# Kernel tuning notes

Hardware: AMD Instinct MI355X
Metric: run time of the kernel (lower is better)

## Reference

```python
import jax, jax.numpy as jnp
import numpy as np

B, N, D, H = 2, 1536, 1024, 16
DH = D // H
SCALE = DH ** -0.5


def setup_inputs() -> dict:
    key = jax.random.key(0)
    ks = jax.random.split(key, 16)
    s = D ** -0.5
    x = jax.random.normal(ks[0], (B, N, D), dtype=jnp.float32)
    # causal prior: 0 on/below diagonal, -1e9 above
    causal = jnp.tril(jnp.ones((N, N), dtype=bool))
    attn_bias = jnp.where(causal, 0.0, -1e9).astype(jnp.float32)[None, None]
    mk = lambda k, shp: jax.random.normal(k, shp, dtype=jnp.float32) * s
    return {
        "x": x,
        "attn_bias": attn_bias,
        "Wq": mk(ks[1], (D, D)), "bq": jnp.zeros((D,), jnp.float32),
        "Wk": mk(ks[2], (D, D)), "bk": jnp.zeros((D,), jnp.float32),
        "Wv": mk(ks[3], (D, D)), "bv": jnp.zeros((D,), jnp.float32),
        "Wg1": mk(ks[4], (D, D)), "bg1": jnp.zeros((D,), jnp.float32),
        "Wg2": mk(ks[5], (D, 1)), "bg2": jnp.zeros((1,), jnp.float32),
        "Wo": mk(ks[6], (D, D)), "bo": jnp.zeros((D,), jnp.float32),
    }


def reference(x, attn_bias, Wq, bq, Wk, bk, Wv, bv, Wg1, bg1, Wg2, bg2, Wo, bo):
    b, n, d = x.shape
    # projections -> [B, H, N, DH]
    split = lambda t: t.reshape(b, n, H, DH).swapaxes(1, 2)
    Q = split(x @ Wq + bq)
    K = split(x @ Wk + bk)
    V = split(x @ Wv + bv)
    # scores [B, H, N, N]
    attn = jnp.einsum("bhnd,bhmd->bhnm", Q, K) * SCALE + attn_bias
    attn = jax.nn.softmax(attn, axis=-1)
    # per-(batch, head, query) entropy over key axis
    entropy = -(attn * jnp.log(attn + 1e-6)).sum(-1)  # [B, H, N]
    # gate MLP (torch nn.GELU default is exact erf)
    gate = jax.nn.sigmoid(jax.nn.gelu(x @ Wg1 + bg1, approximate=False) @ Wg2 + bg2)  # [B, N, 1]
    attn = attn * gate[:, None, :, :]  # broadcast over heads, keys
    out = jnp.einsum("bhnm,bhmd->bhnd", attn, V)
    out = out.swapaxes(1, 2).reshape(b, n, d) @ Wo + bo
    return out, entropy
```

## Files before the change

### kernel.cpp

```cpp
#include <hip/hip_runtime.h>
#include <hip/hip_bf16.h>
#include <math.h>

#define Bsz  2
#define Nseq 1536
#define Dmod 1024
#define NH   16
#define DHd  64
#define MTOT (Bsz*Nseq)
#define SCALE 0.125f
#define BK   32

typedef short  short8 __attribute__((ext_vector_type(8)));
typedef float  f32x4  __attribute__((ext_vector_type(4)));
typedef unsigned short u16x4 __attribute__((ext_vector_type(4)));
typedef unsigned short ushortT;

__device__ __forceinline__ float b2f(__hip_bfloat16 v) { return __bfloat162float(v); }
__device__ __forceinline__ unsigned short f2bf(float f) {
    union { float f; unsigned u; } a; a.f = f;
    unsigned r = a.u + 0x7fffu + ((a.u >> 16) & 1u);
    return (unsigned short)(r >> 16);
}

__device__ __forceinline__ void gl2lds16(const ushortT* g, ushortT* lds) {
    __builtin_amdgcn_global_load_lds(
        (const __attribute__((address_space(1))) unsigned int*)(g),
        (__attribute__((address_space(3))) unsigned int*)(lds),
        16, 0, 0);
}

__global__ __launch_bounds__(256)
void prep_kernel(const float* W0, const float* W1, const float* W2,
                 const float* W3, const float* W4,
                 ushortT* T0, ushortT* T1, ushortT* T2, ushortT* T3, ushortT* T4,
                 const float* __restrict__ x, ushortT* __restrict__ xb,
                 float* __restrict__ glogit)
{
    const int z = blockIdx.z;
    const int t = threadIdx.x;
    if (z == 5) {
        const int bi = blockIdx.y * 16 + blockIdx.x;
        const size_t NEl = (size_t)MTOT * Dmod;
        for (size_t i = ((size_t)bi * 256 + t) * 4; i < NEl; i += (size_t)256 * 256 * 4) {
            float4 v = *(const float4*)(x + i);
            u16x4 o = { f2bf(v.x), f2bf(v.y), f2bf(v.z), f2bf(v.w) };
            *(u16x4*)(xb + i) = o;
        }
        if (t < 12) glogit[bi * 12 + t] = 0.f;
        return;
    }
    __shared__ float tile[64][65];
    const float* W = z == 0 ? W0 : z == 1 ? W1 : z == 2 ? W2 : z == 3 ? W3 : W4;
    ushortT*     T = z == 0 ? T0 : z == 1 ? T1 : z == 2 ? T2 : z == 3 ? T3 : T4;
    const int k0 = blockIdx.x * 64, n0 = blockIdx.y * 64;
    for (int i = t; i < 4096; i += 256) {
        int r = i >> 6, c = i & 63;
        tile[r][c] = W[(size_t)(k0 + r) * 1024 + n0 + c];
    }
    __syncthreads();
    for (int i = t; i < 4096; i += 256) {
        int rn = i >> 6, ck = i & 63;
        T[(size_t)(n0 + rn) * 1024 + k0 + ck] = f2bf(tile[ck][rn]);
    }
}

__device__ __forceinline__
void gemm_core(const ushortT* __restrict__ A, const ushortT* __restrict__ Bt,
               int m0, int n0, ushortT* AsU, ushortT* BsU, f32x4 (&acc)[4][4])
{
    const int t = threadIdx.x;
    const int l = t & 63, w = t >> 6;
    const int wm = (w >> 1) * 64, wn = (w & 1) * 64;
    const int lm = l & 15, q = l >> 4;

    const int r0 = t >> 2, c0 = (t & 3) * 8;
    const ushortT* Ag0 = A  + (size_t)(m0 + r0) * 1024 + c0;
    const ushortT* Ag1 = Ag0 + (size_t)64 * 1024;
    const ushortT* Bg0 = Bt + (size_t)(n0 + r0) * 1024 + c0;
    const ushortT* Bg1 = Bg0 + (size_t)64 * 1024;
    ushortT* La0 = AsU + t * 8;
    ushortT* La1 = AsU + 2048 + t * 8;
    ushortT* Lb0 = BsU + t * 8;
    ushortT* Lb1 = BsU + 2048 + t * 8;

    for (int k0 = 0; k0 < 1024; k0 += BK) {
        gl2lds16(Ag0 + k0, La0);
        gl2lds16(Ag1 + k0, La1);
        gl2lds16(Bg0 + k0, Lb0);
        gl2lds16(Bg1 + k0, Lb1);
        __syncthreads();
        short8 af[4], bf[4];
#pragma unroll
        for (int i = 0; i < 4; ++i) {
            af[i] = *(const short8*)&AsU[(wm + i * 16 + lm) * 32 + q * 8];
            bf[i] = *(const short8*)&BsU[(wn + i * 16 + lm) * 32 + q * 8];
        }
#pragma unroll
        for (int i = 0; i < 4; ++i)
#pragma unroll
            for (int j = 0; j < 4; ++j)
                acc[i][j] = __builtin_amdgcn_mfma_f32_16x16x32_bf16(af[i], bf[j], acc[i][j], 0, 0, 0);
        __syncthreads();
    }
}

__global__ __launch_bounds__(256)
void gemm_qkvg(const ushortT* __restrict__ xb,
               const ushortT* Wt0, const ushortT* Wt1, const ushortT* Wt2, const ushortT* Wt3,
               const float* bz0, const float* bz1, const float* bz2, const float* bz3,
               const float* __restrict__ Wg2,
               ushortT* O0, ushortT* O1, ushortT* O2, float* __restrict__ glogit)
{
    __shared__ ushortT AsU[128 * 32];
    __shared__ ushortT BsU[128 * 32];
    const int z = blockIdx.z;
    const ushortT* Wt  = z == 0 ? Wt0 : z == 1 ? Wt1 : z == 2 ? Wt2 : Wt3;
    const float*  bias = z == 0 ? bz0 : z == 1 ? bz1 : z == 2 ? bz2 : bz3;
    const int m0 = blockIdx.y * 128, n0 = blockIdx.x * 128;

    f32x4 acc[4][4] = {};
    gemm_core(xb, Wt, m0, n0, AsU, BsU, acc);

    const int t = threadIdx.x, l = t & 63, w = t >> 6;
    const int wm = (w >> 1) * 64, wn = (w & 1) * 64;
    const int lm = l & 15, q = l >> 4;

    if (z == 3) {
        float part[4][4] = {};
#pragma unroll
        for (int i = 0; i < 4; ++i)
#pragma unroll
            for (int j = 0; j < 4; ++j) {
                int n = n0 + wn + j * 16 + lm;
                float bn = bias[n];
                float w2 = Wg2[n];
#pragma unroll
                for (int r = 0; r < 4; ++r) {
                    float v = acc[i][j][r] + bn;
                    v = 0.5f * v * (1.0f + erff(v * 0.70710678118654752f));
                    part[i][r] += v * w2;
                }
            }
#pragma unroll
        for (int i = 0; i < 4; ++i)
#pragma unroll
            for (int r = 0; r < 4; ++r) {
                float p = part[i][r];
#pragma unroll
                for (int msk = 1; msk < 16; msk <<= 1) p += __shfl_xor(p, msk, 16);
                if (lm == 0)
                    atomicAdd(&glogit[m0 + wm + i * 16 + q * 4 + r], p);
            }
        return;
    }

    ushortT* O = z == 0 ? O0 : z == 1 ? O1 : O2;
#pragma unroll
    for (int i = 0; i < 4; ++i)
#pragma unroll
        for (int j = 0; j < 4; ++j) {
            int n = n0 + wn + j * 16 + lm;
            float bn = bias[n];
#pragma unroll
            for (int r = 0; r < 4; ++r) {
                int m = m0 + wm + i * 16 + q * 4 + r;
                float v = acc[i][j][r] + bn;
                if (z == 0) v *= SCALE;
                if (z == 2) {
                    int b = m / Nseq, nn = m - b * Nseq;
                    int h = n >> 6, dd = n & 63;
                    O[(size_t)((b * 16 + h) * 64 + dd) * Nseq + nn] = f2bf(v);
                } else {
                    O[(size_t)m * 1024 + n] = f2bf(v);
                }
            }
        }
}

__global__ __launch_bounds__(256)
void gemm_out(const ushortT* __restrict__ AO, const ushortT* __restrict__ WtO,
              const float* __restrict__ bias, float* __restrict__ C)
{
    __shared__ ushortT AsU[128 * 32];
    __shared__ ushortT BsU[128 * 32];
    const int m0 = blockIdx.y * 128, n0 = blockIdx.x * 128;

    f32x4 acc[4][4] = {};
    gemm_core(AO, WtO, m0, n0, AsU, BsU, acc);

    const int t = threadIdx.x, l = t & 63, w = t >> 6;
    const int wm = (w >> 1) * 64, wn = (w & 1) * 64;
    const int lm = l & 15, q = l >> 4;
#pragma unroll
    for (int i = 0; i < 4; ++i)
#pragma unroll
        for (int j = 0; j < 4; ++j) {
            int n = n0 + wn + j * 16 + lm;
            float bn = bias[n];
#pragma unroll
            for (int r = 0; r < 4; ++r) {
                int m = m0 + wm + i * 16 + q * 4 + r;
                C[(size_t)m * 1024 + n] = acc[i][j][r] + bn;
            }
        }
}

__global__ __launch_bounds__(64)
void attn_mfma(const ushortT* __restrict__ Q, const ushortT* __restrict__ K,
               const ushortT* __restrict__ Vt, const float* __restrict__ glogit,
               const float* __restrict__ bg2, ushortT* __restrict__ AO,
               float* __restrict__ ent)
{
    __shared__ ushortT Ps[32][72];

    const int l  = threadIdx.x;
    const int ln = l & 15, q4 = l >> 4;
    const int bh = blockIdx.x, b = bh >> 4, h = bh & 15;
    const int q32 = (int)gridDim.y - 1 - (int)blockIdx.y;
    const int wq = q32 * 32;
    const int kd = wq >> 6;
    const int sbmax = ((wq >> 4) & 3) + 1;

    const ushortT* Qp = Q + (size_t)(b * Nseq + wq + ln) * Dmod + h * DHd + q4 * 8;
    short8 qf[2][2];
    qf[0][0] = *(const short8*)(Qp);
    qf[0][1] = *(const short8*)(Qp + 32);
    qf[1][0] = *(const short8*)(Qp + (size_t)16 * Dmod);
    qf[1][1] = *(const short8*)(Qp + (size_t)16 * Dmod + 32);

    float l_lane[2][4] = {}, t_lane[2][4] = {};
    f32x4 oacc[2][4] = {};

    const ushortT* Kbase = K  + (size_t)(b * Nseq) * Dmod + h * DHd + q4 * 8;
    const ushortT* Vbase = Vt + ((size_t)(b * 16 + h) * 64) * Nseq + q4 * 8;

    short8 kc[4][2];
    {
        const ushortT* Kp = Kbase + (size_t)ln * Dmod;
#pragma unroll
        for (int nb = 0; nb < 4; ++nb) {
            kc[nb][0] = *(const short8*)(Kp + (size_t)nb * 16 * Dmod);
            kc[nb][1] = *(const short8*)(Kp + (size_t)nb * 16 * Dmod + 32);
        }
    }

    for (int kt = 0; kt < kd; ++kt) {
        const int k0 = kt * 64;
        const ushortT* Vp = Vbase + (size_t)ln * Nseq + k0;
        short8 vf[4][2];
#pragma unroll
        for (int nb = 0; nb < 4; ++nb) {
            vf[nb][0] = *(const short8*)(Vp + (size_t)nb * 16 * Nseq);
            vf[nb][1] = *(const short8*)(Vp + (size_t)nb * 16 * Nseq + 32);
        }
        short8 kn[4][2];
        {
            const ushortT* Kp = Kbase + (size_t)(k0 + 64 + ln) * Dmod;
#pragma unroll
            for (int nb = 0; nb < 4; ++nb) {
                kn[nb][0] = *(const short8*)(Kp + (size_t)nb * 16 * Dmod);
                kn[nb][1] = *(const short8*)(Kp + (size_t)nb * 16 * Dmod + 32);
            }
        }
        f32x4 sacc[2][4];
#pragma unroll
        for (int g = 0; g < 2; ++g)
#pragma unroll
            for (int nb = 0; nb < 4; ++nb) {
                f32x4 a = {};
                a = __builtin_amdgcn_mfma_f32_16x16x32_bf16(qf[g][0], kc[nb][0], a, 0, 0, 0);
                a = __builtin_amdgcn_mfma_f32_16x16x32_bf16(qf[g][1], kc[nb][1], a, 0, 0, 0);
                sacc[g][nb] = a;
            }
#pragma unroll
        for (int g = 0; g < 2; ++g)
#pragma unroll
            for (int nb = 0; nb < 4; ++nb)
#pragma unroll
                for (int r = 0; r < 4; ++r) {
                    float sv = sacc[g][nb][r];
                    float ev = __expf(sv);
                    l_lane[g][r] += ev;
                    t_lane[g][r] += ev * sv;
                    Ps[g * 16 + q4 * 4 + r][nb * 16 + ln] = f2bf(ev);
                }
        short8 pf[2][2];
#pragma unroll
        for (int g = 0; g < 2; ++g) {
            pf[g][0] = *(const short8*)&Ps[g * 16 + ln][q4 * 8];
            pf[g][1] = *(const short8*)&Ps[g * 16 + ln][32 + q4 * 8];
        }
#pragma unroll
        for (int g = 0; g < 2; ++g)
#pragma unroll
            for (int nb = 0; nb < 4; ++nb) {
                oacc[g][nb] = __builtin_amdgcn_mfma_f32_16x16x32_bf16(pf[g][0], vf[nb][0], oacc[g][nb], 0, 0, 0);
                oacc[g][nb] = __builtin_amdgcn_mfma_f32_16x16x32_bf16(pf[g][1], vf[nb][1], oacc[g][nb], 0, 0, 0);
            }
#pragma unroll
        for (int nb = 0; nb < 4; ++nb) { kc[nb][0] = kn[nb][0]; kc[nb][1] = kn[nb][1]; }
    }

    {
        const int k0 = kd * 64;
        const ushortT* Vp = Vbase + (size_t)ln * Nseq + k0;
        short8 vf[4][2];
#pragma unroll
        for (int nb = 0; nb < 4; ++nb) {
            vf[nb][0] = *(const short8*)(Vp + (size_t)nb * 16 * Nseq);
            vf[nb][1] = *(const short8*)(Vp + (size_t)nb * 16 * Nseq + 32);
        }
        f32x4 sacc[2][4];
#pragma unroll
        for (int g = 0; g < 2; ++g)
#pragma unroll
            for (int nb = 0; nb < 4; ++nb)
                if (nb <= sbmax) {
                    f32x4 a = {};
                    a = __builtin_amdgcn_mfma_f32_16x16x32_bf16(qf[g][0], kc[nb][0], a, 0, 0, 0);
                    a = __builtin_amdgcn_mfma_f32_16x16x32_bf16(qf[g][1], kc[nb][1], a, 0, 0, 0);
                    sacc[g][nb] = a;
                }
#pragma unroll
        for (int g = 0; g < 2; ++g)
#pragma unroll
            for (int nb = 0; nb < 4; ++nb)
#pragma unroll
                for (int r = 0; r < 4; ++r) {
                    float ev = 0.f;
                    if (nb <= sbmax) {
                        int kg = k0 + nb * 16 + ln;
                        int qg = wq + g * 16 + q4 * 4 + r;
                        float sv = sacc[g][nb][r];
                        ev = (kg <= qg) ? __expf(sv) : 0.f;
                        l_lane[g][r] += ev;
                        t_lane[g][r] += ev * sv;
                    }
                    Ps[g * 16 + q4 * 4 + r][nb * 16 + ln] = f2bf(ev);
                }
        short8 pf[2][2];
#pragma unroll
        for (int g = 0; g < 2; ++g) {
            pf[g][0] = *(const short8*)&Ps[g * 16 + ln][q4 * 8];
            pf[g][1] = *(const short8*)&Ps[g * 16 + ln][32 + q4 * 8];
        }
#pragma unroll
        for (int g = 0; g < 2; ++g)
#pragma unroll
            for (int nb = 0; nb < 4; ++nb) {
                oacc[g][nb] = __builtin_amdgcn_mfma_f32_16x16x32_bf16(pf[g][0], vf[nb][0], oacc[g][nb], 0, 0, 0);
                oacc[g][nb] = __builtin_amdgcn_mfma_f32_16x16x32_bf16(pf[g][1], vf[nb][1], oacc[g][nb], 0, 0, 0);
            }
    }

    const float bg2v = bg2[0];
#pragma unroll
    for (int g = 0; g < 2; ++g) {
        float sc[4];
#pragma unroll
        for (int r = 0; r < 4; ++r) {
            float lv = l_lane[g][r], tv = t_lane[g][r];
#pragma unroll
            for (int msk = 1; msk < 16; msk <<= 1) {
                lv += __shfl_xor(lv, msk, 16);
                tv += __shfl_xor(tv, msk, 16);
            }
            int qg = wq + g * 16 + q4 * 4 + r;
            float inv = 1.f / lv;
            if (ln == 0)
                ent[((size_t)b * NH + h) * Nseq + qg] = logf(lv) - tv * inv;
            float logit = glogit[b * Nseq + qg] + bg2v;
            sc[r] = inv / (1.f + __expf(-logit));
        }
#pragma unroll
        for (int nb = 0; nb < 4; ++nb)
#pragma unroll
            for (int r = 0; r < 4; ++r) {
                int qg = wq + g * 16 + q4 * 4 + r;
                AO[(size_t)(b * Nseq + qg) * Dmod + h * DHd + nb * 16 + ln] =
                    f2bf(oacc[g][nb][r] * sc[r]);
            }
    }
}

extern "C" void kernel_launch(void* const* d_in, const int* in_sizes, int n_in,
                              void* d_out, int out_size, void* d_ws, size_t ws_size,
                              hipStream_t stream)
{
    const float* x   = (const float*)d_in[0];
    const float* Wq  = (const float*)d_in[2];
    const float* bq  = (const float*)d_in[3];
    const float* Wk  = (const float*)d_in[4];
    const float* bk  = (const float*)d_in[5];
    const float* Wv  = (const float*)d_in[6];
    const float* bv  = (const float*)d_in[7];
    const float* Wg1 = (const float*)d_in[8];
    const float* bg1 = (const float*)d_in[9];
    const float* Wg2 = (const float*)d_in[10];
    const float* bg2 = (const float*)d_in[11];
    const float* Wo  = (const float*)d_in[12];
    const float* bo  = (const float*)d_in[13];

    const size_t NE = (size_t)MTOT * Dmod;
    ushortT* p   = (ushortT*)d_ws;
    ushortT* Qw  = p; p += NE;
    ushortT* Kw  = p; p += NE;
    ushortT* Vtw = p; p += NE;
    ushortT* AO  = p; p += NE;
    ushortT* xb  = p; p += NE;
    ushortT* WtQ = p; p += (size_t)1024 * 1024;
    ushortT* WtK = p; p += (size_t)1024 * 1024;
    ushortT* WtV = p; p += (size_t)1024 * 1024;
    ushortT* WtG = p; p += (size_t)1024 * 1024;
    ushortT* WtO = p; p += (size_t)1024 * 1024;
    float* glogit = (float*)p;

    float* out_f = (float*)d_out;
    float* ent_f = out_f + NE;

    prep_kernel<<<dim3(16, 16, 6), 256, 0, stream>>>(Wq, Wk, Wv, Wg1, Wo,
                                                     WtQ, WtK, WtV, WtG, WtO,
                                                     x, xb, glogit);
    gemm_qkvg<<<dim3(8, 24, 4), 256, 0, stream>>>(xb, WtQ, WtK, WtV, WtG,
                                                  bq, bk, bv, bg1, Wg2,
                                                  Qw, Kw, Vtw, glogit);
    attn_mfma<<<dim3(Bsz * NH, Nseq / 32), 64, 0, stream>>>(Qw, Kw, Vtw, glogit,
                                                            bg2, AO, ent_f);
    gemm_out<<<dim3(8, 24), 256, 0, stream>>>(AO, WtO, bo, out_f);
}
```

Baseline: 263.7 us.

## Double-buffer GEMM LDS tiles and shrink N tile to 64 for more blocks

The shared GEMM core now double-buffers the A and B tiles in LDS. It issues the next k-slice's global-to-LDS loads before computing on the current slice, which removes one barrier per iteration. The block tile narrows from 128x128 to 128x64, doubling the grid for both the QKV/gate GEMM and the output GEMM. This is meant to overlap memory with MFMA work and fill more CUs. In exchange each block reuses less data per A tile and the total A-tile traffic doubles.

```diff
diff --git a/kernel.cpp b/kernel.cpp
--- a/kernel.cpp
+++ b/kernel.cpp
@@ -67,41 +67,49 @@
 
 __device__ __forceinline__
 void gemm_core(const ushortT* __restrict__ A, const ushortT* __restrict__ Bt,
-               int m0, int n0, ushortT* AsU, ushortT* BsU, f32x4 (&acc)[4][4])
+               int m0, int n0, ushortT* As, ushortT* Bs, f32x4 (&acc)[4][2])
 {
     const int t = threadIdx.x;
     const int l = t & 63, w = t >> 6;
-    const int wm = (w >> 1) * 64, wn = (w & 1) * 64;
+    const int wm = (w >> 1) * 64, wn = (w & 1) * 32;
     const int lm = l & 15, q = l >> 4;
 
     const int r0 = t >> 2, c0 = (t & 3) * 8;
     const ushortT* Ag0 = A  + (size_t)(m0 + r0) * 1024 + c0;
     const ushortT* Ag1 = Ag0 + (size_t)64 * 1024;
     const ushortT* Bg0 = Bt + (size_t)(n0 + r0) * 1024 + c0;
-    const ushortT* Bg1 = Bg0 + (size_t)64 * 1024;
-    ushortT* La0 = AsU + t * 8;
-    ushortT* La1 = AsU + 2048 + t * 8;
-    ushortT* Lb0 = BsU + t * 8;
-    ushortT* Lb1 = BsU + 2048 + t * 8;
-
-    for (int k0 = 0; k0 < 1024; k0 += BK) {
-        gl2lds16(Ag0 + k0, La0);
-        gl2lds16(Ag1 + k0, La1);
-        gl2lds16(Bg0 + k0, Lb0);
-        gl2lds16(Bg1 + k0, Lb1);
+    ushortT* La0 = As + t * 8;
+    ushortT* La1 = As + 2048 + t * 8;
+    ushortT* Lb0 = Bs + t * 8;
+
+    gl2lds16(Ag0, La0);
+    gl2lds16(Ag1, La1);
+    gl2lds16(Bg0, Lb0);
+
+    for (int kt = 0; kt < 1024 / BK; ++kt) {
         __syncthreads();
-        short8 af[4], bf[4];
-#pragma unroll
-        for (int i = 0; i < 4; ++i) {
-            af[i] = *(const short8*)&AsU[(wm + i * 16 + lm) * 32 + q * 8];
-            bf[i] = *(const short8*)&BsU[(wn + i * 16 + lm) * 32 + q * 8];
-        }
+        if (kt + 1 < 1024 / BK) {
+            int ko = (kt + 1) * BK;
+            int bo = ((kt + 1) & 1) ? 4096 : 0;
+            int bo2 = ((kt + 1) & 1) ? 2048 : 0;
+            gl2lds16(Ag0 + ko, La0 + bo);
+            gl2lds16(Ag1 + ko, La1 + bo);
+            gl2lds16(Bg0 + ko, Lb0 + bo2);
+        }
+        const ushortT* Ab = As + ((kt & 1) ? 4096 : 0);
+        const ushortT* Bb = Bs + ((kt & 1) ? 2048 : 0);
+        short8 af[4], bf[2];
 #pragma unroll
         for (int i = 0; i < 4; ++i)
-#pragma unroll
-            for (int j = 0; j < 4; ++j)
+            af[i] = *(const short8*)&Ab[(wm + i * 16 + lm) * 32 + q * 8];
+#pragma unroll
+        for (int j = 0; j < 2; ++j)
+            bf[j] = *(const short8*)&Bb[(wn + j * 16 + lm) * 32 + q * 8];
+#pragma unroll
+        for (int i = 0; i < 4; ++i)
+#pragma unroll
+            for (int j = 0; j < 2; ++j)
                 acc[i][j] = __builtin_amdgcn_mfma_f32_16x16x32_bf16(af[i], bf[j], acc[i][j], 0, 0, 0);
-        __syncthreads();
     }
 }
 
@@ -112,18 +120,18 @@
                const float* __restrict__ Wg2,
                ushortT* O0, ushortT* O1, ushortT* O2, float* __restrict__ glogit)
 {
-    __shared__ ushortT AsU[128 * 32];
-    __shared__ ushortT BsU[128 * 32];
+    __shared__ ushortT As[2 * 128 * 32];
+    __shared__ ushortT Bs[2 * 64 * 32];
     const int z = blockIdx.z;
     const ushortT* Wt  = z == 0 ? Wt0 : z == 1 ? Wt1 : z == 2 ? Wt2 : Wt3;
     const float*  bias = z == 0 ? bz0 : z == 1 ? bz1 : z == 2 ? bz2 : bz3;
-    const int m0 = blockIdx.y * 128, n0 = blockIdx.x * 128;
-
-    f32x4 acc[4][4] = {};
-    gemm_core(xb, Wt, m0, n0, AsU, BsU, acc);
+    const int m0 = blockIdx.y * 128, n0 = blockIdx.x * 64;
+
+    f32x4 acc[4][2] = {};
+    gemm_core(xb, Wt, m0, n0, As, Bs, acc);
 
     const int t = threadIdx.x, l = t & 63, w = t >> 6;
-    const int wm = (w >> 1) * 64, wn = (w & 1) * 64;
+    const int wm = (w >> 1) * 64, wn = (w & 1) * 32;
     const int lm = l & 15, q = l >> 4;
 
     if (z == 3) {
@@ -131,7 +139,7 @@
 #pragma unroll
         for (int i = 0; i < 4; ++i)
 #pragma unroll
-            for (int j = 0; j < 4; ++j) {
+            for (int j = 0; j < 2; ++j) {
                 int n = n0 + wn + j * 16 + lm;
                 float bn = bias[n];
                 float w2 = Wg2[n];
@@ -159,7 +167,7 @@
 #pragma unroll
     for (int i = 0; i < 4; ++i)
 #pragma unroll
-        for (int j = 0; j < 4; ++j) {
+        for (int j = 0; j < 2; ++j) {
             int n = n0 + wn + j * 16 + lm;
             float bn = bias[n];
 #pragma unroll
@@ -182,20 +190,20 @@
 void gemm_out(const ushortT* __restrict__ AO, const ushortT* __restrict__ WtO,
               const float* __restrict__ bias, float* __restrict__ C)
 {
-    __shared__ ushortT AsU[128 * 32];
-    __shared__ ushortT BsU[128 * 32];
-    const int m0 = blockIdx.y * 128, n0 = blockIdx.x * 128;
-
-    f32x4 acc[4][4] = {};
-    gemm_core(AO, WtO, m0, n0, AsU, BsU, acc);
+    __shared__ ushortT As[2 * 128 * 32];
+    __shared__ ushortT Bs[2 * 64 * 32];
+    const int m0 = blockIdx.y * 128, n0 = blockIdx.x * 64;
+
+    f32x4 acc[4][2] = {};
+    gemm_core(AO, WtO, m0, n0, As, Bs, acc);
 
     const int t = threadIdx.x, l = t & 63, w = t >> 6;
-    const int wm = (w >> 1) * 64, wn = (w & 1) * 64;
+    const int wm = (w >> 1) * 64, wn = (w & 1) * 32;
     const int lm = l & 15, q = l >> 4;
 #pragma unroll
     for (int i = 0; i < 4; ++i)
 #pragma unroll
-        for (int j = 0; j < 4; ++j) {
+        for (int j = 0; j < 2; ++j) {
             int n = n0 + wn + j * 16 + lm;
             float bn = bias[n];
 #pragma unroll
@@ -422,10 +430,10 @@
     prep_kernel<<<dim3(16, 16, 6), 256, 0, stream>>>(Wq, Wk, Wv, Wg1, Wo,
                                                      WtQ, WtK, WtV, WtG, WtO,
                                                      x, xb, glogit);
-    gemm_qkvg<<<dim3(8, 24, 4), 256, 0, stream>>>(xb, WtQ, WtK, WtV, WtG,
-                                                  bq, bk, bv, bg1, Wg2,
-                                                  Qw, Kw, Vtw, glogit);
+    gemm_qkvg<<<dim3(16, 24, 4), 256, 0, stream>>>(xb, WtQ, WtK, WtV, WtG,
+                                                   bq, bk, bv, bg1, Wg2,
+                                                   Qw, Kw, Vtw, glogit);
     attn_mfma<<<dim3(Bsz * NH, Nseq / 32), 64, 0, stream>>>(Qw, Kw, Vtw, glogit,
                                                             bg2, AO, ent_f);
-    gemm_out<<<dim3(8, 24), 256, 0, stream>>>(AO, WtO, bo, out_f);
-}
+    gemm_out<<<dim3(16, 24), 256, 0, stream>>>(AO, WtO, bo, out_f);
+}
```

Result: faster. 234.0 us (-11.3%).
